# Kernel tuning notes

Measured on AMD Instinct MI355X. Metric: run time of the kernel, lower is better.

Reference implementation:

```python
import jax, jax.numpy as jnp
import numpy as np

H = 16          # num_heads
EPS = 1e-6      # RMSNorm eps


def _rms_norm(t, w):
    # t: [..., head_dim], w: [head_dim]
    var = jnp.mean(jnp.square(t), axis=-1, keepdims=True)
    return t * jax.lax.rsqrt(var + EPS) * w


def setup_inputs() -> dict:
    key = jax.random.key(0)
    ks = jax.random.split(key, 8)
    B, N, M, C = 2, 2048, 256, 1024
    s = 0.02
    return {
        "x": jax.random.normal(ks[0], (B, N, C), jnp.float32),
        "y": jax.random.normal(ks[1], (B, M, C), jnp.float32),
        "qkv_w": jax.random.normal(ks[2], (3 * C, C), jnp.float32) * s,
        "qkv_b": jax.random.normal(ks[3], (3 * C,), jnp.float32) * s,
        "kv_w": jax.random.normal(ks[4], (2 * C, C), jnp.float32) * s,
        "kv_b": jax.random.normal(ks[5], (2 * C,), jnp.float32) * s,
        "qn_w": jnp.ones((C // H,), jnp.float32),
        "kn_w": jnp.ones((C // H,), jnp.float32),
        "proj_w": jax.random.normal(ks[6], (C, C), jnp.float32) * s,
        "proj_b": jax.random.normal(ks[7], (C,), jnp.float32) * s,
    }


def reference(x, y, qkv_w, qkv_b, kv_w, kv_b, qn_w, kn_w, proj_w, proj_b):
    B, N, C = x.shape
    M = y.shape[1]
    hd = C // H
    scale = hd ** -0.5

    # fused QKV projection for image tokens -> [B, H, N, hd] each
    qkv = (jnp.einsum('bnc,oc->bno', x, qkv_w) + qkv_b).reshape(B, N, 3, H, hd)
    qkv = jnp.transpose(qkv, (2, 0, 3, 1, 4))
    q, kx, vx = qkv[0], qkv[1], qkv[2]

    # qk-norm (RMSNorm over head_dim)
    q = _rms_norm(q, qn_w)
    kx = _rms_norm(kx, kn_w)

    # KV projection for text tokens -> [B, H, M, hd] each
    kvy = (jnp.einsum('bmc,oc->bmo', y, kv_w) + kv_b).reshape(B, M, 2, H, hd)
    kvy = jnp.transpose(kvy, (2, 0, 3, 1, 4))
    ky, vy = kvy[0], kvy[1]
    ky = _rms_norm(ky, kn_w)

    # concat image+text KV along the sequence axis
    k = jnp.concatenate([kx, ky], axis=2)  # [B, H, N+M, hd]
    v = jnp.concatenate([vx, vy], axis=2)

    # scaled dot-product attention
    logits = jnp.einsum('bhnd,bhsd->bhns', q, k) * scale  # [B, H, N, N+M]
    attn = jax.nn.softmax(logits, axis=-1)
    out = jnp.einsum('bhns,bhsd->bhnd', attn, v)          # [B, H, N, hd]

    out = jnp.transpose(out, (0, 2, 1, 3)).reshape(B, N, C)
    return jnp.einsum('bnc,oc->bno', out, proj_w) + proj_b
```

## Files before the change

kernel.cpp:

```cpp
#include <hip/hip_runtime.h>

#define BATCH 2
#define NTOK 2048
#define MTOK 256
#define CDIM 1024
#define NHEAD 16
#define HD 64
#define SEQ (NTOK + MTOK)
#define TOK_X (BATCH * NTOK)
#define TOK_Y (BATCH * MTOK)
#define BHN (BATCH * NHEAD)
#define NKT (SEQ / 64)

typedef __attribute__((ext_vector_type(8))) short bf16x8;
typedef __attribute__((ext_vector_type(4))) short bf16x4;
typedef __attribute__((ext_vector_type(4))) float f32x4;
typedef __attribute__((ext_vector_type(2))) unsigned int u32x2;
typedef __attribute__((ext_vector_type(4))) unsigned int u32x4;
#if __has_builtin(__builtin_amdgcn_cvt_pk_bf16_f32)
typedef __attribute__((ext_vector_type(2))) __bf16 bf16x2_t;
#endif

__device__ __forceinline__ float b2f(ushort u) {
    unsigned v = ((unsigned)u) << 16;
    return __builtin_bit_cast(float, v);
}
__device__ __forceinline__ ushort f2b(float f) {
    unsigned u = __builtin_bit_cast(unsigned, f);
    u += 0x7fffu + ((u >> 16) & 1u);
    return (ushort)(u >> 16);
}
__device__ __forceinline__ unsigned pack2bf(float a, float b) {
#if __has_builtin(__builtin_amdgcn_cvt_pk_bf16_f32)
    bf16x2_t h = __builtin_amdgcn_cvt_pk_bf16_f32(a, b);
    return __builtin_bit_cast(unsigned, h);
#else
    return ((unsigned)f2b(b) << 16) | (unsigned)f2b(a);
#endif
}

__device__ __forceinline__ void async_load16(const ushort* g, ushort* l) {
    __builtin_amdgcn_global_load_lds(
        (const __attribute__((address_space(1))) unsigned*)(const void*)g,
        (__attribute__((address_space(3))) unsigned*)(void*)l, 16, 0, 0);
}

__global__ __launch_bounds__(256) void cast_all(
    const float* __restrict__ s0, ushort* __restrict__ t0, int b0,
    const float* __restrict__ s1, ushort* __restrict__ t1, int b1,
    const float* __restrict__ s2, ushort* __restrict__ t2, int b2,
    const float* __restrict__ s3, ushort* __restrict__ t3, int b3,
    const float* __restrict__ s4, ushort* __restrict__ t4) {
    int blk = blockIdx.x;
    const float* s; ushort* t;
    if (blk < b0)      { s = s0; t = t0; }
    else if (blk < b1) { s = s1; t = t1; blk -= b0; }
    else if (blk < b2) { s = s2; t = t2; blk -= b1; }
    else if (blk < b3) { s = s3; t = t3; blk -= b2; }
    else               { s = s4; t = t4; blk -= b3; }
    int i = (blk * 256 + threadIdx.x) * 8;
    float4 a = *(const float4*)(s + i);
    float4 b = *(const float4*)(s + i + 4);
    ushort tmp[8] = {f2b(a.x), f2b(a.y), f2b(a.z), f2b(a.w),
                     f2b(b.x), f2b(b.y), f2b(b.z), f2b(b.w)};
    *(uint4*)(t + i) = *(const uint4*)tmp;
}

template <int MODE>
__global__ __launch_bounds__(256) void gemm_fused(const ushort* __restrict__ A,
                                                  const ushort* __restrict__ Bt,
                                                  const float* __restrict__ bias,
                                                  float* __restrict__ Cf,
                                                  ushort* __restrict__ d_q,
                                                  ushort* __restrict__ d_k,
                                                  ushort* __restrict__ d_v,
                                                  const float* __restrict__ qn_w,
                                                  const float* __restrict__ kn_w,
                                                  int M, int N, int K) {
    __shared__ ushort As[128][64];
    __shared__ ushort Bs[128][64];
    int tid = threadIdx.x;
    int lane = tid & 63;
    int w = tid >> 6;
    int wm = (w >> 1) * 64;
    int wn = (w & 1) * 64;
    int l15 = lane & 15;
    int quad = lane >> 4;
    int sw = l15 & 7;

    int bx, by;
    if (MODE == 2) {
        bx = blockIdx.x; by = blockIdx.y;
    } else {
        int xcd = blockIdx.x & 7;
        int loc = blockIdx.x >> 3;
        by = xcd * 4 + (loc & 3);
        bx = loc >> 2;
    }
    int bm = by * 128;
    int bn = bx * 128;

    f32x4 acc[4][4];
#pragma unroll
    for (int i = 0; i < 4; i++)
#pragma unroll
        for (int j = 0; j < 4; j++) acc[i][j] = (f32x4)0.0f;

    int lrow = lane >> 3;
    int lcol = ((lane & 7) ^ lrow) * 8;

    for (int k0 = 0; k0 < K; k0 += 64) {
        __syncthreads();
#pragma unroll
        for (int p = 0; p < 4; p++) {
            int rb = w * 32 + p * 8;
            async_load16(&A[(size_t)(bm + rb + lrow) * K + k0 + lcol], &As[rb][0]);
            async_load16(&Bt[(size_t)(bn + rb + lrow) * K + k0 + lcol], &Bs[rb][0]);
        }
        __syncthreads();
#pragma unroll
        for (int kk = 0; kk < 64; kk += 32) {
            bf16x8 af[4], bfr[4];
            int g = (kk >> 3) + quad;
            int csw = (g ^ sw) * 8;
#pragma unroll
            for (int i = 0; i < 4; i++)
                af[i] = *(const bf16x8*)&As[wm + i * 16 + l15][csw];
#pragma unroll
            for (int j = 0; j < 4; j++)
                bfr[j] = *(const bf16x8*)&Bs[wn + j * 16 + l15][csw];
#pragma unroll
            for (int i = 0; i < 4; i++)
#pragma unroll
                for (int j = 0; j < 4; j++)
                    acc[i][j] = __builtin_amdgcn_mfma_f32_16x16x32_bf16(af[i], bfr[j], acc[i][j], 0, 0, 0);
        }
    }

    int colbase = bn + wn;
    float bv[4];
#pragma unroll
    for (int j = 0; j < 4; j++) bv[j] = bias[colbase + j * 16 + l15];
#pragma unroll
    for (int i = 0; i < 4; i++)
#pragma unroll
        for (int j = 0; j < 4; j++)
#pragma unroll
            for (int r = 0; r < 4; r++) acc[i][j][r] += bv[j];

    if (MODE == 0) {
#pragma unroll
        for (int i = 0; i < 4; i++) {
            int row0 = bm + wm + i * 16 + quad * 4;
#pragma unroll
            for (int j = 0; j < 4; j++) {
                int col = colbase + j * 16 + l15;
#pragma unroll
                for (int r = 0; r < 4; r++)
                    Cf[(size_t)(row0 + r) * N + col] = acc[i][j][r];
            }
        }
        return;
    }

    int region = colbase >> 10;
    int h = (colbase >> 6) & (NHEAD - 1);
    bool do_norm = (MODE == 1) ? (region <= 1) : (region == 0);
    if (do_norm) {
        const float* wv = (MODE == 1 && region == 0) ? qn_w : kn_w;
        float wj[4];
#pragma unroll
        for (int j = 0; j < 4; j++) wj[j] = wv[j * 16 + l15];
        float qs = (MODE == 1 && region == 0) ? (0.125f * 1.44269504088896f) : 1.0f;
#pragma unroll
        for (int i = 0; i < 4; i++)
#pragma unroll
            for (int r = 0; r < 4; r++) {
                float s = acc[i][0][r] * acc[i][0][r] + acc[i][1][r] * acc[i][1][r]
                        + acc[i][2][r] * acc[i][2][r] + acc[i][3][r] * acc[i][3][r];
                s += __shfl_xor(s, 1);
                s += __shfl_xor(s, 2);
                s += __shfl_xor(s, 4);
                s += __shfl_xor(s, 8);
                float rs = rsqrtf(s * (1.0f / 64.0f) + 1e-6f) * qs;
#pragma unroll
                for (int j = 0; j < 4; j++) acc[i][j][r] *= rs * wj[j];
            }
    }
#pragma unroll
    for (int i = 0; i < 4; i++) {
#pragma unroll
        for (int r = 0; r < 4; r++) {
            int t = bm + wm + i * 16 + quad * 4 + r;
            size_t base;
            ushort* dst;
            if (MODE == 1) {
                int b = t >> 11, n = t & (NTOK - 1);
                size_t bh = (size_t)(b * NHEAD + h);
                if (region == 0)      { dst = d_q; base = (bh * NTOK + n) * 64; }
                else if (region == 1) { dst = d_k; base = (bh * SEQ + n) * 64; }
                else                  { dst = d_v; base = (bh * SEQ + n) * 64; }
            } else {
                int b = t >> 8, m = t & (MTOK - 1);
                size_t bh = (size_t)(b * NHEAD + h);
                if (region == 0) { dst = d_k; base = (bh * SEQ + NTOK + m) * 64; }
                else             { dst = d_v; base = (bh * SEQ + NTOK + m) * 64; }
            }
#pragma unroll
            for (int j = 0; j < 4; j++)
                dst[base + j * 16 + l15] = f2b(acc[i][j][r]);
        }
    }
}

__global__ __launch_bounds__(256) void transpose_v(const ushort* __restrict__ vc,
                                                   ushort* __restrict__ vt) {
    __shared__ ushort t[64][72];
    int bh = blockIdx.y;
    int s0 = blockIdx.x * 64;
    int tid = threadIdx.x;
    int r = tid >> 3, c = (tid & 7) * 8;
    const ushort* src = vc + ((size_t)bh * SEQ + s0) * 64;
    *(uint4*)&t[r][c] = *(const uint4*)&src[(size_t)r * 64 + c];
    *(uint4*)&t[r + 32][c] = *(const uint4*)&src[(size_t)(r + 32) * 64 + c];
    __syncthreads();
    ushort* dst = vt + (size_t)bh * 64 * SEQ + s0;
#pragma unroll
    for (int p = 0; p < 2; p++) {
        int d = (tid >> 3) + p * 32;
        int s8 = (tid & 7) * 8;
        ushort tmp[8];
#pragma unroll
        for (int i = 0; i < 8; i++) {
            int cc = s8 + i;
            int srcs = (cc & 32) + ((cc & 31) >> 1) + ((cc & 1) << 4);
            tmp[i] = t[srcs][d];
        }
        *(uint4*)&dst[(size_t)d * SEQ + s8] = *(const uint4*)tmp;
    }
}

__global__ __launch_bounds__(256) void attn_fwd(const ushort* __restrict__ qh,
                                                const ushort* __restrict__ kc,
                                                const ushort* __restrict__ vt,
                                                ushort* __restrict__ out) {
    __shared__ ushort Ks[2][64][72];
    __shared__ ushort Vs[2][64][68];
    int tid = threadIdx.x;
    int lane = tid & 63;
    int w = tid >> 6;
    int l15 = lane & 15;
    int quad = lane >> 4;
    int bh = blockIdx.y;
    int q0 = blockIdx.x * 128 + w * 32;

    const ushort* qpA = qh + ((size_t)bh * NTOK + q0 + l15) * 64 + quad * 8;
    const ushort* qpB = qpA + 16 * 64;
    bf16x8 qA0 = *(const bf16x8*)qpA;
    bf16x8 qA1 = *(const bf16x8*)(qpA + 32);
    bf16x8 qB0 = *(const bf16x8*)qpB;
    bf16x8 qB1 = *(const bf16x8*)(qpB + 32);

    float lA = 0.0f, lB = 0.0f;
    f32x4 OA[4], OB[4];
#pragma unroll
    for (int jd = 0; jd < 4; jd++) { OA[jd] = (f32x4)0.0f; OB[jd] = (f32x4)0.0f; }

    const ushort* kbase = kc + (size_t)bh * SEQ * 64;
    const ushort* vbase = vt + (size_t)bh * 64 * SEQ;
    int sr = tid >> 3, sc = (tid & 7) * 8;
    const ushort* kp0 = kbase + (size_t)sr * 64 + sc;
    const ushort* kp1 = kbase + (size_t)(sr + 32) * 64 + sc;
    const ushort* vp0 = vbase + (size_t)sr * SEQ + sc;
    const ushort* vp1 = vbase + (size_t)(sr + 32) * SEQ + sc;

    uint4 rka = *(const uint4*)kp0;
    uint4 rkb = *(const uint4*)kp1;
    uint4 rva = *(const uint4*)vp0;
    uint4 rvb = *(const uint4*)vp1;

    for (int t = 0; t < NKT; t++) {
        int p = t & 1;
        *(uint4*)&Ks[p][sr][sc] = rka;
        *(uint4*)&Ks[p][sr + 32][sc] = rkb;
        *(uint4*)&Vs[p][sr][sc] = rva;
        *(uint4*)&Vs[p][sr + 32][sc] = rvb;
        __syncthreads();
        if (t + 1 < NKT) {
            int s0 = (t + 1) * 64;
            rka = *(const uint4*)(kp0 + (size_t)s0 * 64);
            rkb = *(const uint4*)(kp1 + (size_t)s0 * 64);
            rva = *(const uint4*)(vp0 + s0);
            rvb = *(const uint4*)(vp1 + s0);
        }

        f32x4 SA[4], SB[4];
#pragma unroll
        for (int j = 0; j < 4; j++) { SA[j] = (f32x4)0.0f; SB[j] = (f32x4)0.0f; }
#pragma unroll
        for (int j = 0; j < 4; j++) {
            bf16x8 kf = *(const bf16x8*)&Ks[p][j * 16 + l15][quad * 8];
            SA[j] = __builtin_amdgcn_mfma_f32_16x16x32_bf16(kf, qA0, SA[j], 0, 0, 0);
            SB[j] = __builtin_amdgcn_mfma_f32_16x16x32_bf16(kf, qB0, SB[j], 0, 0, 0);
        }
#pragma unroll
        for (int j = 0; j < 4; j++) {
            bf16x8 kf = *(const bf16x8*)&Ks[p][j * 16 + l15][32 + quad * 8];
            SA[j] = __builtin_amdgcn_mfma_f32_16x16x32_bf16(kf, qA1, SA[j], 0, 0, 0);
            SB[j] = __builtin_amdgcn_mfma_f32_16x16x32_bf16(kf, qB1, SB[j], 0, 0, 0);
        }

#pragma unroll
        for (int pb2 = 0; pb2 < 2; pb2++) {
            int j0 = 2 * pb2, j1 = j0 + 1;
            u32x4 wa, wb;
#pragma unroll
            for (int r = 0; r < 4; r++) {
                float a0 = __builtin_amdgcn_exp2f(SA[j0][r]);
                float a1 = __builtin_amdgcn_exp2f(SA[j1][r]);
                lA += a0 + a1;
                wa[r] = pack2bf(a0, a1);
                float b0 = __builtin_amdgcn_exp2f(SB[j0][r]);
                float b1 = __builtin_amdgcn_exp2f(SB[j1][r]);
                lB += b0 + b1;
                wb[r] = pack2bf(b0, b1);
            }
            bf16x8 pA = __builtin_bit_cast(bf16x8, wa);
            bf16x8 pB = __builtin_bit_cast(bf16x8, wb);
#pragma unroll
            for (int jd = 0; jd < 4; jd++) {
                bf16x8 vf = *(const bf16x8*)&Vs[p][jd * 16 + l15][pb2 * 32 + quad * 8];
                OA[jd] = __builtin_amdgcn_mfma_f32_16x16x32_bf16(vf, pA, OA[jd], 0, 0, 0);
                OB[jd] = __builtin_amdgcn_mfma_f32_16x16x32_bf16(vf, pB, OB[jd], 0, 0, 0);
            }
        }
    }
    lA += __shfl_xor(lA, 16);
    lA += __shfl_xor(lA, 32);
    lB += __shfl_xor(lB, 16);
    lB += __shfl_xor(lB, 32);
    float invA = 1.0f / lA;
    float invB = 1.0f / lB;
    int b = bh >> 4, h = bh & 15;
    int tokA = (b << 11) + q0 + l15;
    ushort* obaseA = out + ((size_t)tokA * NHEAD + h) * 64;
    ushort* obaseB = obaseA + (size_t)16 * NHEAD * 64;
#pragma unroll
    for (int jd = 0; jd < 4; jd++) {
        u32x2 pk;
        pk.x = pack2bf(OA[jd][0] * invA, OA[jd][1] * invA);
        pk.y = pack2bf(OA[jd][2] * invA, OA[jd][3] * invA);
        *(u32x2*)&obaseA[jd * 16 + quad * 4] = pk;
        pk.x = pack2bf(OB[jd][0] * invB, OB[jd][1] * invB);
        pk.y = pack2bf(OB[jd][2] * invB, OB[jd][3] * invB);
        *(u32x2*)&obaseB[jd * 16 + quad * 4] = pk;
    }
}

extern "C" void kernel_launch(void* const* d_in, const int* in_sizes, int n_in,
                              void* d_out, int out_size, void* d_ws, size_t ws_size,
                              hipStream_t stream) {
    const float* x      = (const float*)d_in[0];
    const float* y      = (const float*)d_in[1];
    const float* qkv_w  = (const float*)d_in[2];
    const float* qkv_b  = (const float*)d_in[3];
    const float* kv_w   = (const float*)d_in[4];
    const float* kv_b   = (const float*)d_in[5];
    const float* qn_w   = (const float*)d_in[6];
    const float* kn_w   = (const float*)d_in[7];
    const float* proj_w = (const float*)d_in[8];
    const float* proj_b = (const float*)d_in[9];
    float* outp = (float*)d_out;

    char* ws = (char*)d_ws;
    ushort* x_bf    = (ushort*)ws; ws += (size_t)TOK_X * CDIM * 2;
    ushort* y_bf    = (ushort*)ws; ws += (size_t)TOK_Y * CDIM * 2;
    ushort* qkvw_bf = (ushort*)ws; ws += (size_t)3 * CDIM * CDIM * 2;
    ushort* kvw_bf  = (ushort*)ws; ws += (size_t)2 * CDIM * CDIM * 2;
    ushort* projw_bf= (ushort*)ws; ws += (size_t)CDIM * CDIM * 2;
    ushort* qh      = (ushort*)ws; ws += (size_t)BHN * NTOK * 64 * 2;
    ushort* kc      = (ushort*)ws; ws += (size_t)BHN * SEQ * 64 * 2;
    ushort* vc      = (ushort*)ws; ws += (size_t)BHN * SEQ * 64 * 2;
    ushort* vt      = (ushort*)ws; ws += (size_t)BHN * SEQ * 64 * 2;
    ushort* ao      = (ushort*)ws; ws += (size_t)TOK_X * CDIM * 2;

    int c0 = TOK_X * CDIM / 2048;
    int c1 = c0 + TOK_Y * CDIM / 2048;
    int c2 = c1 + 3 * CDIM * CDIM / 2048;
    int c3 = c2 + 2 * CDIM * CDIM / 2048;
    int c4 = c3 + CDIM * CDIM / 2048;
    cast_all<<<c4, 256, 0, stream>>>(x, x_bf, c0, y, y_bf, c1, qkv_w, qkvw_bf, c2,
                                     kv_w, kvw_bf, c3, proj_w, projw_bf);

    gemm_fused<1><<<768, 256, 0, stream>>>(
        x_bf, qkvw_bf, qkv_b, nullptr, qh, kc, vc, qn_w, kn_w, TOK_X, 3 * CDIM, CDIM);
    gemm_fused<2><<<dim3(2 * CDIM / 128, TOK_Y / 128), 256, 0, stream>>>(
        y_bf, kvw_bf, kv_b, nullptr, nullptr, kc, vc, qn_w, kn_w, TOK_Y, 2 * CDIM, CDIM);

    transpose_v<<<dim3(SEQ / 64, BHN), 256, 0, stream>>>(vc, vt);

    attn_fwd<<<dim3(NTOK / 128, BHN), 256, 0, stream>>>(qh, kc, vt, ao);

    gemm_fused<0><<<256, 256, 0, stream>>>(
        ao, projw_bf, proj_b, outp, nullptr, nullptr, nullptr, nullptr, nullptr,
        TOK_X, CDIM, CDIM);
}
```

Baseline: 250.5 us.

## Merge QKV and KV GEMMs into one launch and write V pre-transposed

Combines the image QKV projection and text KV projection into a single kernel launch, dispatching on block index. The epilogue now writes V straight into the transposed, permuted layout the attention kernel expects, so the separate transpose kernel and the intermediate V buffer go away. This saves two launches and one full read and write of V, but the transposed epilogue stores are strided by SEQ and scattered, which may coalesce poorly.

```diff
diff --git a/kernel.cpp b/kernel.cpp
--- a/kernel.cpp
+++ b/kernel.cpp
@@ -11,6 +11,8 @@
 #define TOK_Y (BATCH * MTOK)
 #define BHN (BATCH * NHEAD)
 #define NKT (SEQ / 64)
+#define QKV_BLOCKS 768
+#define KV_BLOCKS 64
 
 typedef __attribute__((ext_vector_type(8))) short bf16x8;
 typedef __attribute__((ext_vector_type(4))) short bf16x4;
@@ -66,17 +68,17 @@
     *(uint4*)(t + i) = *(const uint4*)tmp;
 }
 
-template <int MODE>
-__global__ __launch_bounds__(256) void gemm_fused(const ushort* __restrict__ A,
-                                                  const ushort* __restrict__ Bt,
-                                                  const float* __restrict__ bias,
-                                                  float* __restrict__ Cf,
+__global__ __launch_bounds__(256) void gemm_qkvkv(const ushort* __restrict__ Aq,
+                                                  const ushort* __restrict__ Wq,
+                                                  const float* __restrict__ bq,
+                                                  const ushort* __restrict__ Ak,
+                                                  const ushort* __restrict__ Wk,
+                                                  const float* __restrict__ bk,
                                                   ushort* __restrict__ d_q,
                                                   ushort* __restrict__ d_k,
-                                                  ushort* __restrict__ d_v,
+                                                  ushort* __restrict__ d_vt,
                                                   const float* __restrict__ qn_w,
-                                                  const float* __restrict__ kn_w,
-                                                  int M, int N, int K) {
+                                                  const float* __restrict__ kn_w) {
     __shared__ ushort As[128][64];
     __shared__ ushort Bs[128][64];
     int tid = threadIdx.x;
@@ -88,14 +90,23 @@
     int quad = lane >> 4;
     int sw = l15 & 7;
 
-    int bx, by;
-    if (MODE == 2) {
-        bx = blockIdx.x; by = blockIdx.y;
-    } else {
-        int xcd = blockIdx.x & 7;
-        int loc = blockIdx.x >> 3;
+    int blk = blockIdx.x;
+    int mode, bx, by;
+    const ushort *A, *Bt;
+    const float* bias;
+    if (blk < QKV_BLOCKS) {
+        mode = 1;
+        int xcd = blk & 7;
+        int loc = blk >> 3;
         by = xcd * 4 + (loc & 3);
         bx = loc >> 2;
+        A = Aq; Bt = Wq; bias = bq;
+    } else {
+        mode = 2;
+        int loc = blk - QKV_BLOCKS;
+        bx = loc & 15;
+        by = loc >> 4;
+        A = Ak; Bt = Wk; bias = bk;
     }
     int bm = by * 128;
     int bn = bx * 128;
@@ -109,13 +120,13 @@
     int lrow = lane >> 3;
     int lcol = ((lane & 7) ^ lrow) * 8;
 
-    for (int k0 = 0; k0 < K; k0 += 64) {
+    for (int k0 = 0; k0 < CDIM; k0 += 64) {
         __syncthreads();
 #pragma unroll
         for (int p = 0; p < 4; p++) {
             int rb = w * 32 + p * 8;
-            async_load16(&A[(size_t)(bm + rb + lrow) * K + k0 + lcol], &As[rb][0]);
-            async_load16(&Bt[(size_t)(bn + rb + lrow) * K + k0 + lcol], &Bs[rb][0]);
+            async_load16(&A[(size_t)(bm + rb + lrow) * CDIM + k0 + lcol], &As[rb][0]);
+            async_load16(&Bt[(size_t)(bn + rb + lrow) * CDIM + k0 + lcol], &Bs[rb][0]);
         }
         __syncthreads();
 #pragma unroll
@@ -148,30 +159,16 @@
 #pragma unroll
             for (int r = 0; r < 4; r++) acc[i][j][r] += bv[j];
 
-    if (MODE == 0) {
-#pragma unroll
-        for (int i = 0; i < 4; i++) {
-            int row0 = bm + wm + i * 16 + quad * 4;
-#pragma unroll
-            for (int j = 0; j < 4; j++) {
-                int col = colbase + j * 16 + l15;
-#pragma unroll
-                for (int r = 0; r < 4; r++)
-                    Cf[(size_t)(row0 + r) * N + col] = acc[i][j][r];
-            }
-        }
-        return;
-    }
-
     int region = colbase >> 10;
     int h = (colbase >> 6) & (NHEAD - 1);
-    bool do_norm = (MODE == 1) ? (region <= 1) : (region == 0);
-    if (do_norm) {
-        const float* wv = (MODE == 1 && region == 0) ? qn_w : kn_w;
+    bool is_q = (mode == 1) && (region == 0);
+    bool is_k = (mode == 1) ? (region == 1) : (region == 0);
+    if (is_q || is_k) {
+        const float* wv = is_q ? qn_w : kn_w;
         float wj[4];
 #pragma unroll
         for (int j = 0; j < 4; j++) wj[j] = wv[j * 16 + l15];
-        float qs = (MODE == 1 && region == 0) ? (0.125f * 1.44269504088896f) : 1.0f;
+        float qs = is_q ? (0.125f * 1.44269504088896f) : 1.0f;
 #pragma unroll
         for (int i = 0; i < 4; i++)
 #pragma unroll
@@ -187,56 +184,106 @@
                 for (int j = 0; j < 4; j++) acc[i][j][r] *= rs * wj[j];
             }
     }
+    size_t l15seq = (size_t)l15 * SEQ;
 #pragma unroll
     for (int i = 0; i < 4; i++) {
 #pragma unroll
         for (int r = 0; r < 4; r++) {
             int t = bm + wm + i * 16 + quad * 4 + r;
-            size_t base;
-            ushort* dst;
-            if (MODE == 1) {
-                int b = t >> 11, n = t & (NTOK - 1);
-                size_t bh = (size_t)(b * NHEAD + h);
-                if (region == 0)      { dst = d_q; base = (bh * NTOK + n) * 64; }
-                else if (region == 1) { dst = d_k; base = (bh * SEQ + n) * 64; }
-                else                  { dst = d_v; base = (bh * SEQ + n) * 64; }
+            int b, s;
+            if (mode == 1) { b = t >> 11; s = t & (NTOK - 1); }
+            else           { b = t >> 8;  s = NTOK + (t & (MTOK - 1)); }
+            size_t bh = (size_t)(b * NHEAD + h);
+            if (is_q) {
+                size_t base = (bh * NTOK + s) * 64;
+#pragma unroll
+                for (int j = 0; j < 4; j++)
+                    d_q[base + j * 16 + l15] = f2b(acc[i][j][r]);
+            } else if (is_k) {
+                size_t base = (bh * SEQ + s) * 64;
+#pragma unroll
+                for (int j = 0; j < 4; j++)
+                    d_k[base + j * 16 + l15] = f2b(acc[i][j][r]);
             } else {
-                int b = t >> 8, m = t & (MTOK - 1);
-                size_t bh = (size_t)(b * NHEAD + h);
-                if (region == 0) { dst = d_k; base = (bh * SEQ + NTOK + m) * 64; }
-                else             { dst = d_v; base = (bh * SEQ + NTOK + m) * 64; }
+                int within = s & 31;
+                int pos = ((s >> 5) << 5) + ((within & 15) << 1) + (within >> 4);
+                size_t base = bh * 64 * SEQ + l15seq + pos;
+#pragma unroll
+                for (int j = 0; j < 4; j++)
+                    d_vt[base + (size_t)(j * 16) * SEQ] = f2b(acc[i][j][r]);
             }
+        }
+    }
+}
+
+__global__ __launch_bounds__(256) void gemm_proj(const ushort* __restrict__ A,
+                                                 const ushort* __restrict__ Bt,
+                                                 const float* __restrict__ bias,
+                                                 float* __restrict__ Cf) {
+    __shared__ ushort As[128][64];
+    __shared__ ushort Bs[128][64];
+    int tid = threadIdx.x;
+    int lane = tid & 63;
+    int w = tid >> 6;
+    int wm = (w >> 1) * 64;
+    int wn = (w & 1) * 64;
+    int l15 = lane & 15;
+    int quad = lane >> 4;
+    int sw = l15 & 7;
+    int xcd = blockIdx.x & 7;
+    int loc = blockIdx.x >> 3;
+    int by = xcd * 4 + (loc & 3);
+    int bx = loc >> 2;
+    int bm = by * 128;
+    int bn = bx * 128;
+
+    f32x4 acc[4][4];
+#pragma unroll
+    for (int i = 0; i < 4; i++)
+#pragma unroll
+        for (int j = 0; j < 4; j++) acc[i][j] = (f32x4)0.0f;
+
+    int lrow = lane >> 3;
+    int lcol = ((lane & 7) ^ lrow) * 8;
+
+    for (int k0 = 0; k0 < CDIM; k0 += 64) {
+        __syncthreads();
+#pragma unroll
+        for (int p = 0; p < 4; p++) {
+            int rb = w * 32 + p * 8;
+            async_load16(&A[(size_t)(bm + rb + lrow) * CDIM + k0 + lcol], &As[rb][0]);
+            async_load16(&Bt[(size_t)(bn + rb + lrow) * CDIM + k0 + lcol], &Bs[rb][0]);
+        }
+        __syncthreads();
+#pragma unroll
+        for (int kk = 0; kk < 64; kk += 32) {
+            bf16x8 af[4], bfr[4];
+            int g = (kk >> 3) + quad;
+            int csw = (g ^ sw) * 8;
+#pragma unroll
+            for (int i = 0; i < 4; i++)
+                af[i] = *(const bf16x8*)&As[wm + i * 16 + l15][csw];
 #pragma unroll
             for (int j = 0; j < 4; j++)
-                dst[base + j * 16 + l15] = f2b(acc[i][j][r]);
-        }
-    }
-}
-
-__global__ __launch_bounds__(256) void transpose_v(const ushort* __restrict__ vc,
-                                                   ushort* __restrict__ vt) {
-    __shared__ ushort t[64][72];
-    int bh = blockIdx.y;
-    int s0 = blockIdx.x * 64;
-    int tid = threadIdx.x;
-    int r = tid >> 3, c = (tid & 7) * 8;
-    const ushort* src = vc + ((size_t)bh * SEQ + s0) * 64;
-    *(uint4*)&t[r][c] = *(const uint4*)&src[(size_t)r * 64 + c];
-    *(uint4*)&t[r + 32][c] = *(const uint4*)&src[(size_t)(r + 32) * 64 + c];
-    __syncthreads();
-    ushort* dst = vt + (size_t)bh * 64 * SEQ + s0;
-#pragma unroll
-    for (int p = 0; p < 2; p++) {
-        int d = (tid >> 3) + p * 32;
-        int s8 = (tid & 7) * 8;
-        ushort tmp[8];
-#pragma unroll
-        for (int i = 0; i < 8; i++) {
-            int cc = s8 + i;
-            int srcs = (cc & 32) + ((cc & 31) >> 1) + ((cc & 1) << 4);
-            tmp[i] = t[srcs][d];
-        }
-        *(uint4*)&dst[(size_t)d * SEQ + s8] = *(const uint4*)tmp;
+                bfr[j] = *(const bf16x8*)&Bs[wn + j * 16 + l15][csw];
+#pragma unroll
+            for (int i = 0; i < 4; i++)
+#pragma unroll
+                for (int j = 0; j < 4; j++)
+                    acc[i][j] = __builtin_amdgcn_mfma_f32_16x16x32_bf16(af[i], bfr[j], acc[i][j], 0, 0, 0);
+        }
+    }
+#pragma unroll
+    for (int i = 0; i < 4; i++) {
+        int row0 = bm + wm + i * 16 + quad * 4;
+#pragma unroll
+        for (int j = 0; j < 4; j++) {
+            int col = bn + wn + j * 16 + l15;
+            float bvv = bias[col];
+#pragma unroll
+            for (int r = 0; r < 4; r++)
+                Cf[(size_t)(row0 + r) * CDIM + col] = acc[i][j][r] + bvv;
+        }
     }
 }
 
@@ -266,13 +313,11 @@
 #pragma unroll
     for (int jd = 0; jd < 4; jd++) { OA[jd] = (f32x4)0.0f; OB[jd] = (f32x4)0.0f; }
 
-    const ushort* kbase = kc + (size_t)bh * SEQ * 64;
-    const ushort* vbase = vt + (size_t)bh * 64 * SEQ;
     int sr = tid >> 3, sc = (tid & 7) * 8;
-    const ushort* kp0 = kbase + (size_t)sr * 64 + sc;
-    const ushort* kp1 = kbase + (size_t)(sr + 32) * 64 + sc;
-    const ushort* vp0 = vbase + (size_t)sr * SEQ + sc;
-    const ushort* vp1 = vbase + (size_t)(sr + 32) * SEQ + sc;
+    const ushort* kp0 = kc + (size_t)bh * SEQ * 64 + (size_t)sr * 64 + sc;
+    const ushort* kp1 = kp0 + (size_t)32 * 64;
+    const ushort* vp0 = vt + (size_t)bh * 64 * SEQ + (size_t)sr * SEQ + sc;
+    const ushort* vp1 = vp0 + (size_t)32 * SEQ;
 
     uint4 rka = *(const uint4*)kp0;
     uint4 rkb = *(const uint4*)kp1;
@@ -287,11 +332,11 @@
         *(uint4*)&Vs[p][sr + 32][sc] = rvb;
         __syncthreads();
         if (t + 1 < NKT) {
-            int s0 = (t + 1) * 64;
-            rka = *(const uint4*)(kp0 + (size_t)s0 * 64);
-            rkb = *(const uint4*)(kp1 + (size_t)s0 * 64);
-            rva = *(const uint4*)(vp0 + s0);
-            rvb = *(const uint4*)(vp1 + s0);
+            kp0 += 64 * 64; kp1 += 64 * 64; vp0 += 64; vp1 += 64;
+            rka = *(const uint4*)kp0;
+            rkb = *(const uint4*)kp1;
+            rva = *(const uint4*)vp0;
+            rvb = *(const uint4*)vp1;
         }
 
         f32x4 SA[4], SB[4];
@@ -380,7 +425,6 @@
     ushort* projw_bf= (ushort*)ws; ws += (size_t)CDIM * CDIM * 2;
     ushort* qh      = (ushort*)ws; ws += (size_t)BHN * NTOK * 64 * 2;
     ushort* kc      = (ushort*)ws; ws += (size_t)BHN * SEQ * 64 * 2;
-    ushort* vc      = (ushort*)ws; ws += (size_t)BHN * SEQ * 64 * 2;
     ushort* vt      = (ushort*)ws; ws += (size_t)BHN * SEQ * 64 * 2;
     ushort* ao      = (ushort*)ws; ws += (size_t)TOK_X * CDIM * 2;
 
@@ -392,16 +436,10 @@
     cast_all<<<c4, 256, 0, stream>>>(x, x_bf, c0, y, y_bf, c1, qkv_w, qkvw_bf, c2,
                                      kv_w, kvw_bf, c3, proj_w, projw_bf);
 
-    gemm_fused<1><<<768, 256, 0, stream>>>(
-        x_bf, qkvw_bf, qkv_b, nullptr, qh, kc, vc, qn_w, kn_w, TOK_X, 3 * CDIM, CDIM);
-    gemm_fused<2><<<dim3(2 * CDIM / 128, TOK_Y / 128), 256, 0, stream>>>(
-        y_bf, kvw_bf, kv_b, nullptr, nullptr, kc, vc, qn_w, kn_w, TOK_Y, 2 * CDIM, CDIM);
-
-    transpose_v<<<dim3(SEQ / 64, BHN), 256, 0, stream>>>(vc, vt);
+    gemm_qkvkv<<<QKV_BLOCKS + KV_BLOCKS, 256, 0, stream>>>(
+        x_bf, qkvw_bf, qkv_b, y_bf, kvw_bf, kv_b, qh, kc, vt, qn_w, kn_w);
 
     attn_fwd<<<dim3(NTOK / 128, BHN), 256, 0, stream>>>(qh, kc, vt, ao);
 
-    gemm_fused<0><<<256, 256, 0, stream>>>(
-        ao, projw_bf, proj_b, outp, nullptr, nullptr, nullptr, nullptr, nullptr,
-        TOK_X, CDIM, CDIM);
-}
+    gemm_proj<<<256, 256, 0, stream>>>(ao, projw_bf, proj_b, outp);
+}
```

Result: faster. 240.1 us (-4.1%).
